# Kernel tuning notes

Measured on AMD Instinct MI355X. Metric: run time of the kernel, lower is better.

Reference implementation:

```python
import jax, jax.numpy as jnp
import numpy as np

N, F, H = 512, 256, 512

def _w(k, i, o):
    return jax.random.normal(k, (i, o), jnp.float32) * (1.0 / np.sqrt(i))

def setup_inputs() -> dict:
    key = jax.random.key(0)
    ks = jax.random.split(key, 12)
    z = lambda n: jnp.zeros((n,), jnp.float32)
    return {
        "node_features": jax.random.normal(ks[0], (N, F), jnp.float32),
        "adjacency": jax.random.uniform(ks[1], (N, N), jnp.float32),
        # GraphConv layers: neighbor linear (wl,bl) and self-loop (ws,bs)
        "gc1_wl": _w(ks[2], F, H), "gc1_bl": z(H), "gc1_ws": _w(ks[3], F, H), "gc1_bs": z(H),
        "gc2_wl": _w(ks[4], H, H), "gc2_bl": z(H), "gc2_ws": _w(ks[5], H, H), "gc2_bs": z(H),
        "gc3_wl": _w(ks[6], H, F), "gc3_bl": z(F), "gc3_ws": _w(ks[7], H, F), "gc3_bs": z(F),
        # edge MLP: Linear(2F,H) -> ReLU -> (dropout=identity, eval) -> Linear(H,H) -> ReLU -> Linear(H,1)
        "mlp_w1": _w(ks[8], 2 * F, H), "mlp_b1": z(H),
        "mlp_w2": _w(ks[9], H, H), "mlp_b2": z(H),
        "mlp_w3": _w(ks[10], H, 1), "mlp_b3": z(1),
    }

def _gconv(x, adj_norm, wl, bl, ws, bs):
    # adj_norm @ Linear(x) + SelfLoop(x)
    return adj_norm @ (x @ wl + bl) + (x @ ws + bs)

def reference(node_features, adjacency,
              gc1_wl, gc1_bl, gc1_ws, gc1_bs,
              gc2_wl, gc2_bl, gc2_ws, gc2_bs,
              gc3_wl, gc3_bl, gc3_ws, gc3_bs,
              mlp_w1, mlp_b1, mlp_w2, mlp_b2, mlp_w3, mlp_b3):
    # row-normalized adjacency (shared across all three layers)
    adj_norm = adjacency / (adjacency.sum(axis=1, keepdims=True) + 1e-8)
    x = jax.nn.relu(_gconv(node_features, adj_norm, gc1_wl, gc1_bl, gc1_ws, gc1_bs))
    x = jax.nn.relu(_gconv(x, adj_norm, gc2_wl, gc2_bl, gc2_ws, gc2_bs))
    emb = _gconv(x, adj_norm, gc3_wl, gc3_bl, gc3_ws, gc3_bs)  # [N, F]
    # vectorized all-pairs (i<j) edge scoring, symmetric scatter
    iu, ju = np.triu_indices(N, k=1)  # static index lists, P = N(N-1)/2
    ef = jnp.concatenate([emb[iu], emb[ju]], axis=-1)  # [P, 2F]
    h = jax.nn.relu(ef @ mlp_w1 + mlp_b1)
    h = jax.nn.relu(h @ mlp_w2 + mlp_b2)
    s = jax.nn.sigmoid((h @ mlp_w3 + mlp_b3)[:, 0])  # [P]
    edge_scores = jnp.zeros((N, N), emb.dtype).at[iu, ju].set(s).at[ju, iu].set(s)
    return emb, edge_scores
```

## Files before the change

### kernel.cpp

```cpp
#include <hip/hip_runtime.h>
#include <hip/hip_bf16.h>


#define NN 512
#define FF 256
#define HH 512

typedef __attribute__((ext_vector_type(8))) short s8v;
typedef __attribute__((ext_vector_type(4))) float f4v;

__device__ __forceinline__ ushort f2bf(float f) {
  unsigned u = __float_as_uint(f);
  unsigned r = (u + 0x7fffu + ((u >> 16) & 1u)) >> 16;
  return (ushort)r;
}

__global__ __launch_bounds__(256)
void rownorm_kernel(const float* __restrict__ adj, float* __restrict__ adjn) {
  int row = blockIdx.x;
  int tid = threadIdx.x;
  const float* r = adj + row * NN;
  float a0 = r[tid], a1 = r[tid + 256];
  float s = a0 + a1;
#pragma unroll
  for (int m = 1; m < 64; m <<= 1) s += __shfl_xor(s, m);
  __shared__ float wsum[4];
  if ((tid & 63) == 0) wsum[tid >> 6] = s;
  __syncthreads();
  float inv = 1.f / (wsum[0] + wsum[1] + wsum[2] + wsum[3] + 1e-8f);
  float* o = adjn + row * NN;
  o[tid] = a0 * inv;
  o[tid + 256] = a1 * inv;
}

template <bool RELU>
__global__ __launch_bounds__(256)
void gemm_ts(int M, int N, int K,
             const float* __restrict__ A, int lda,
             const float* __restrict__ B0, const float* __restrict__ B1, int ldb,
             const float* __restrict__ bias0, const float* __restrict__ bias1,
             const float* __restrict__ add0, const float* __restrict__ add1, int ldadd,
             float* __restrict__ C0, float* __restrict__ C1, int ldc)
{
  const float* B = blockIdx.z ? B1 : B0;
  const float* bias = blockIdx.z ? bias1 : bias0;
  const float* add = blockIdx.z ? add1 : add0;
  float* C = blockIdx.z ? C1 : C0;
  const int n0 = blockIdx.x * 64;
  const int m0 = blockIdx.y * 16;
  const int tid = threadIdx.x;
  const int ty = tid >> 4, tx = tid & 15;

  __shared__ float As[32][18];
  __shared__ float Bs[32][68];
  float4 acc = {0.f, 0.f, 0.f, 0.f};

  const int am = tid >> 4;
  const int ak = tid & 15;
  const int bk = tid >> 4;
  const int bn = tid & 15;

  float2 pa = *(const float2*)&A[(m0 + am) * lda + ak * 2];
  float4 pb0 = *(const float4*)&B[bk * ldb + n0 + bn * 4];
  float4 pb1 = *(const float4*)&B[(bk + 16) * ldb + n0 + bn * 4];

  for (int k0 = 0; k0 < K; k0 += 32) {
    As[ak * 2][am] = pa.x;
    As[ak * 2 + 1][am] = pa.y;
    *(float4*)&Bs[bk][bn * 4] = pb0;
    *(float4*)&Bs[bk + 16][bn * 4] = pb1;
    __syncthreads();
    if (k0 + 32 < K) {
      pa = *(const float2*)&A[(m0 + am) * lda + k0 + 32 + ak * 2];
      pb0 = *(const float4*)&B[(k0 + 32 + bk) * ldb + n0 + bn * 4];
      pb1 = *(const float4*)&B[(k0 + 48 + bk) * ldb + n0 + bn * 4];
    }
#pragma unroll
    for (int k = 0; k < 32; ++k) {
      float a = As[k][ty];
      float4 b = *(const float4*)&Bs[k][tx * 4];
      acc.x += a * b.x; acc.y += a * b.y; acc.z += a * b.z; acc.w += a * b.w;
    }
    __syncthreads();
  }

  int m = m0 + ty;
  float4 v = acc;
  if (bias) {
    float4 bv = *(const float4*)&bias[n0 + tx * 4];
    v.x += bv.x; v.y += bv.y; v.z += bv.z; v.w += bv.w;
  }
  if (add) {
    float4 d = *(const float4*)&add[m * ldadd + n0 + tx * 4];
    v.x += d.x; v.y += d.y; v.z += d.z; v.w += d.w;
  }
  if (RELU) {
    v.x = fmaxf(v.x, 0.f); v.y = fmaxf(v.y, 0.f);
    v.z = fmaxf(v.z, 0.f); v.w = fmaxf(v.w, 0.f);
  }
  *(float4*)&C[m * ldc + n0 + tx * 4] = v;
}

__global__ __launch_bounds__(256)
void w2_pack(const float* __restrict__ w2, ushort* __restrict__ w2t2) {
  int slab = blockIdx.y;
  int col = blockIdx.x * 64 + (threadIdx.x >> 2);
  int kq = threadIdx.x & 3;
  int k0 = slab * 32 + kq * 8;
  ushort tmp[8];
#pragma unroll
  for (int e = 0; e < 8; ++e) tmp[e] = f2bf(w2[(k0 + e) * HH + col]);
  ushort* dst = w2t2 + slab * 16384 + col * 32 + kq * 8;
  *(ushort4*)dst = *(ushort4*)tmp;
  *(ushort4*)(dst + 4) = *(ushort4*)&tmp[4];
}

__global__ __launch_bounds__(512)
__attribute__((amdgpu_waves_per_eu(2, 2)))
void edge_mlp(const float* __restrict__ Amat, const float* __restrict__ Bmat,
              const ushort* __restrict__ w2t2,
              const float* __restrict__ b2, const float* __restrict__ w3,
              const float* __restrict__ b3,
              float* __restrict__ edges)
{
  __shared__ ushort h1s[2][128 * 128];
  __shared__ float part[8][640];

  const int tb = (int)blockIdx.x;
  int bj = (int)((sqrtf(4.f * tb + 1.f) - 1.f) * 0.5f);
  while (bj * bj + bj > tb) --bj;
  while ((bj + 1) * (bj + 2) <= tb) ++bj;
  const int bi = tb - bj * bj - bj;

  const int tid = threadIdx.x;
  const int wid = tid >> 6;
  const int lane = tid & 63;
  const int l15 = lane & 15;
  const int lg = lane >> 4;

  const f4v zero = {0.f, 0.f, 0.f, 0.f};
  f4v acc[8][4];
#pragma unroll
  for (int mf = 0; mf < 8; ++mf)
#pragma unroll
    for (int nf = 0; nf < 4; ++nf) acc[mf][nf] = zero;

  auto stage = [&](int ch, int buf) {
#pragma unroll 2
    for (int q = 0; q < 8; ++q) {
      int fidx = q * 512 + tid;
      int p = fidx >> 5;
      int k4 = fidx & 31;
      int i = bi * 8 + (p >> 4);
      int j = bj * 16 + (p & 15);
      float4 av = *(const float4*)(Amat + i * HH + ch * 128 + k4 * 4);
      float4 bv = *(const float4*)(Bmat + j * HH + ch * 128 + k4 * 4);
      ushort4 pk;
      pk.x = f2bf(fmaxf(av.x + bv.x, 0.f));
      pk.y = f2bf(fmaxf(av.y + bv.y, 0.f));
      pk.z = f2bf(fmaxf(av.z + bv.z, 0.f));
      pk.w = f2bf(fmaxf(av.w + bv.w, 0.f));
      int off = (p * 256 + k4 * 8) ^ ((p & 7) << 4);
      *(ushort4*)((char*)h1s[buf] + off) = pk;
    }
  };

  stage(0, 0);
  __syncthreads();

  const ushort* wbase = w2t2 + wid * 2048 + l15 * 32 + lg * 8;

  for (int ch = 0; ch < 4; ++ch) {
    int cur = ch & 1;
    if (ch < 3) stage(ch + 1, cur ^ 1);
    s8v nb0, nb1, nb2, nb3;
    {
      const ushort* wb = wbase + (ch * 4) * 16384;
      nb0 = *(const s8v*)wb;
      nb1 = *(const s8v*)(wb + 512);
      nb2 = *(const s8v*)(wb + 1024);
      nb3 = *(const s8v*)(wb + 1536);
    }
#pragma unroll
    for (int ks = 0; ks < 4; ++ks) {
      s8v cb0 = nb0, cb1 = nb1, cb2 = nb2, cb3 = nb3;
      if (ks < 3) {
        const ushort* wb = wbase + (ch * 4 + ks + 1) * 16384;
        nb0 = *(const s8v*)wb;
        nb1 = *(const s8v*)(wb + 512);
        nb2 = *(const s8v*)(wb + 1024);
        nb3 = *(const s8v*)(wb + 1536);
      }
#pragma unroll
      for (int mf = 0; mf < 8; ++mf) {
        int p = mf * 16 + l15;
        int off = (p * 256 + ks * 64 + lg * 16) ^ ((p & 7) << 4);
        s8v a = *(const s8v*)((const char*)h1s[cur] + off);
        acc[mf][0] = __builtin_amdgcn_mfma_f32_16x16x32_bf16(a, cb0, acc[mf][0], 0, 0, 0);
        acc[mf][1] = __builtin_amdgcn_mfma_f32_16x16x32_bf16(a, cb1, acc[mf][1], 0, 0, 0);
        acc[mf][2] = __builtin_amdgcn_mfma_f32_16x16x32_bf16(a, cb2, acc[mf][2], 0, 0, 0);
        acc[mf][3] = __builtin_amdgcn_mfma_f32_16x16x32_bf16(a, cb3, acc[mf][3], 0, 0, 0);
      }
    }
    __syncthreads();
  }

  float bb[4], ww[4];
#pragma unroll
  for (int nf = 0; nf < 4; ++nf) {
    int col = wid * 64 + nf * 16 + l15;
    bb[nf] = b2[col];
    ww[nf] = w3[col];
  }
#pragma unroll
  for (int mf = 0; mf < 8; ++mf) {
    float ps[4];
#pragma unroll
    for (int e = 0; e < 4; ++e) {
      ps[e] = fmaxf(acc[mf][0][e] + bb[0], 0.f) * ww[0] +
              fmaxf(acc[mf][1][e] + bb[1], 0.f) * ww[1] +
              fmaxf(acc[mf][2][e] + bb[2], 0.f) * ww[2] +
              fmaxf(acc[mf][3][e] + bb[3], 0.f) * ww[3];
    }
#pragma unroll
    for (int m = 1; m < 16; m <<= 1) {
#pragma unroll
      for (int e = 0; e < 4; ++e) ps[e] += __shfl_xor(ps[e], m);
    }
    if (l15 == 0) {
#pragma unroll
      for (int e = 0; e < 4; ++e)
        part[wid][mf * 16 + lg * 4 + e] = ps[e];
    }
  }
  __syncthreads();
  if (tid < 128) {
    float tot = b3[0];
#pragma unroll
    for (int w = 0; w < 8; ++w) tot += part[w][tid];
    float sg = 1.f / (1.f + expf(-tot));
    int i = bi * 8 + (tid >> 4);
    int j = bj * 16 + (tid & 15);
    if (i < j) {
      edges[i * NN + j] = sg;
      edges[j * NN + i] = sg;
    } else if (i == j) {
      edges[i * NN + i] = 0.f;
    }
  }
}

extern "C" void kernel_launch(void* const* d_in, const int* in_sizes, int n_in,
                              void* d_out, int out_size, void* d_ws, size_t ws_size,
                              hipStream_t stream) {
  const float* node = (const float*)d_in[0];
  const float* adj  = (const float*)d_in[1];
  const float* g1wl = (const float*)d_in[2];
  const float* g1bl = (const float*)d_in[3];
  const float* g1ws = (const float*)d_in[4];
  const float* g1bs = (const float*)d_in[5];
  const float* g2wl = (const float*)d_in[6];
  const float* g2bl = (const float*)d_in[7];
  const float* g2ws = (const float*)d_in[8];
  const float* g2bs = (const float*)d_in[9];
  const float* g3wl = (const float*)d_in[10];
  const float* g3bl = (const float*)d_in[11];
  const float* g3ws = (const float*)d_in[12];
  const float* g3bs = (const float*)d_in[13];
  const float* w1 = (const float*)d_in[14];
  const float* b1 = (const float*)d_in[15];
  const float* w2 = (const float*)d_in[16];
  const float* b2 = (const float*)d_in[17];
  const float* w3 = (const float*)d_in[18];
  const float* b3 = (const float*)d_in[19];

  float* out = (float*)d_out;
  float* emb = out;
  float* edges = out + NN * FF;

  char* wsb = (char*)d_ws;
  float* adjn = (float*)wsb;
  float* Tb   = (float*)(wsb + (1u << 20));
  float* Sb   = (float*)(wsb + (2u << 20));
  float* xa   = (float*)(wsb + (3u << 20));
  float* xb   = (float*)(wsb + (4u << 20));
  ushort* w2t2 = (ushort*)(wsb + (5u << 20));
  float* Amat = Tb;
  float* Bmat = Sb;

  rownorm_kernel<<<NN, 256, 0, stream>>>(adj, adjn);
  w2_pack<<<dim3(8, 16), 256, 0, stream>>>(w2, w2t2);

  gemm_ts<false><<<dim3(8, 32, 2), 256, 0, stream>>>(
      NN, HH, FF, node, FF, g1wl, g1ws, HH, g1bl, g1bs,
      nullptr, nullptr, 0, Tb, Sb, HH);
  gemm_ts<true><<<dim3(8, 32, 1), 256, 0, stream>>>(
      NN, HH, NN, adjn, NN, Tb, Tb, HH, nullptr, nullptr,
      Sb, Sb, HH, xa, xa, HH);
  gemm_ts<false><<<dim3(8, 32, 2), 256, 0, stream>>>(
      NN, HH, HH, xa, HH, g2wl, g2ws, HH, g2bl, g2bs,
      nullptr, nullptr, 0, Tb, Sb, HH);
  gemm_ts<true><<<dim3(8, 32, 1), 256, 0, stream>>>(
      NN, HH, NN, adjn, NN, Tb, Tb, HH, nullptr, nullptr,
      Sb, Sb, HH, xb, xb, HH);
  gemm_ts<false><<<dim3(4, 32, 2), 256, 0, stream>>>(
      NN, FF, HH, xb, HH, g3wl, g3ws, FF, g3bl, g3bs,
      nullptr, nullptr, 0, Tb, Sb, FF);
  gemm_ts<false><<<dim3(4, 32, 1), 256, 0, stream>>>(
      NN, FF, NN, adjn, NN, Tb, Tb, FF, nullptr, nullptr,
      Sb, Sb, FF, emb, emb, FF);

  gemm_ts<false><<<dim3(8, 32, 2), 256, 0, stream>>>(
      NN, HH, FF, emb, FF, w1, w1 + FF * HH, HH, b1, nullptr,
      nullptr, nullptr, 0, Amat, Bmat, HH);

  edge_mlp<<<1056, 512, 0, stream>>>(Amat, Bmat, w2t2, b2, w3, b3, edges);
}
```

Before: 208.0 us.

## Split staging of next chunk into halves interleaved with MFMA slabs

The staging of the next h1 chunk (global loads of A/B rows, add+ReLU, bf16 pack, LDS store) is split into two halves. Each half's global loads are issued before two MFMA slab steps and written to LDS afterward, so load latency is hidden behind matrix math. The W2 prefetch now runs as a single chain across all 16 slabs instead of restarting per chunk. The extra float4 staging registers raise register pressure and may lower occupancy.

```diff
diff --git a/kernel.cpp b/kernel.cpp
--- a/kernel.cpp
+++ b/kernel.cpp
@@ -145,63 +145,81 @@
 #pragma unroll
     for (int nf = 0; nf < 4; ++nf) acc[mf][nf] = zero;
 
-  auto stage = [&](int ch, int buf) {
-#pragma unroll 2
-    for (int q = 0; q < 8; ++q) {
-      int fidx = q * 512 + tid;
+  float4 sa[4], sb[4];
+  auto issue_half = [&](int ch, int h) {
+#pragma unroll
+    for (int q = 0; q < 4; ++q) {
+      int fidx = (h * 4 + q) * 512 + tid;
       int p = fidx >> 5;
       int k4 = fidx & 31;
       int i = bi * 8 + (p >> 4);
       int j = bj * 16 + (p & 15);
-      float4 av = *(const float4*)(Amat + i * HH + ch * 128 + k4 * 4);
-      float4 bv = *(const float4*)(Bmat + j * HH + ch * 128 + k4 * 4);
+      sa[q] = *(const float4*)(Amat + i * HH + ch * 128 + k4 * 4);
+      sb[q] = *(const float4*)(Bmat + j * HH + ch * 128 + k4 * 4);
+    }
+  };
+  auto write_half = [&](int buf, int h) {
+#pragma unroll
+    for (int q = 0; q < 4; ++q) {
+      int fidx = (h * 4 + q) * 512 + tid;
+      int p = fidx >> 5;
+      int k4 = fidx & 31;
       ushort4 pk;
-      pk.x = f2bf(fmaxf(av.x + bv.x, 0.f));
-      pk.y = f2bf(fmaxf(av.y + bv.y, 0.f));
-      pk.z = f2bf(fmaxf(av.z + bv.z, 0.f));
-      pk.w = f2bf(fmaxf(av.w + bv.w, 0.f));
+      pk.x = f2bf(fmaxf(sa[q].x + sb[q].x, 0.f));
+      pk.y = f2bf(fmaxf(sa[q].y + sb[q].y, 0.f));
+      pk.z = f2bf(fmaxf(sa[q].z + sb[q].z, 0.f));
+      pk.w = f2bf(fmaxf(sa[q].w + sb[q].w, 0.f));
       int off = (p * 256 + k4 * 8) ^ ((p & 7) << 4);
       *(ushort4*)((char*)h1s[buf] + off) = pk;
     }
   };
 
-  stage(0, 0);
+  issue_half(0, 0); write_half(0, 0);
+  issue_half(0, 1); write_half(0, 1);
   __syncthreads();
 
   const ushort* wbase = w2t2 + wid * 2048 + l15 * 32 + lg * 8;
 
-  for (int ch = 0; ch < 4; ++ch) {
-    int cur = ch & 1;
-    if (ch < 3) stage(ch + 1, cur ^ 1);
-    s8v nb0, nb1, nb2, nb3;
-    {
-      const ushort* wb = wbase + (ch * 4) * 16384;
+  s8v nb0, nb1, nb2, nb3;
+  nb0 = *(const s8v*)wbase;
+  nb1 = *(const s8v*)(wbase + 512);
+  nb2 = *(const s8v*)(wbase + 1024);
+  nb3 = *(const s8v*)(wbase + 1536);
+
+  auto slab_step = [&](int cur, int slab) {
+    s8v cb0 = nb0, cb1 = nb1, cb2 = nb2, cb3 = nb3;
+    if (slab < 15) {
+      const ushort* wb = wbase + (slab + 1) * 16384;
       nb0 = *(const s8v*)wb;
       nb1 = *(const s8v*)(wb + 512);
       nb2 = *(const s8v*)(wb + 1024);
       nb3 = *(const s8v*)(wb + 1536);
     }
-#pragma unroll
-    for (int ks = 0; ks < 4; ++ks) {
-      s8v cb0 = nb0, cb1 = nb1, cb2 = nb2, cb3 = nb3;
-      if (ks < 3) {
-        const ushort* wb = wbase + (ch * 4 + ks + 1) * 16384;
-        nb0 = *(const s8v*)wb;
-        nb1 = *(const s8v*)(wb + 512);
-        nb2 = *(const s8v*)(wb + 1024);
-        nb3 = *(const s8v*)(wb + 1536);
-      }
-#pragma unroll
-      for (int mf = 0; mf < 8; ++mf) {
-        int p = mf * 16 + l15;
-        int off = (p * 256 + ks * 64 + lg * 16) ^ ((p & 7) << 4);
-        s8v a = *(const s8v*)((const char*)h1s[cur] + off);
-        acc[mf][0] = __builtin_amdgcn_mfma_f32_16x16x32_bf16(a, cb0, acc[mf][0], 0, 0, 0);
-        acc[mf][1] = __builtin_amdgcn_mfma_f32_16x16x32_bf16(a, cb1, acc[mf][1], 0, 0, 0);
-        acc[mf][2] = __builtin_amdgcn_mfma_f32_16x16x32_bf16(a, cb2, acc[mf][2], 0, 0, 0);
-        acc[mf][3] = __builtin_amdgcn_mfma_f32_16x16x32_bf16(a, cb3, acc[mf][3], 0, 0, 0);
-      }
-    }
+    int ks = slab & 3;
+#pragma unroll
+    for (int mf = 0; mf < 8; ++mf) {
+      int p = mf * 16 + l15;
+      int off = (p * 256 + ks * 64 + lg * 16) ^ ((p & 7) << 4);
+      s8v a = *(const s8v*)((const char*)h1s[cur] + off);
+      acc[mf][0] = __builtin_amdgcn_mfma_f32_16x16x32_bf16(a, cb0, acc[mf][0], 0, 0, 0);
+      acc[mf][1] = __builtin_amdgcn_mfma_f32_16x16x32_bf16(a, cb1, acc[mf][1], 0, 0, 0);
+      acc[mf][2] = __builtin_amdgcn_mfma_f32_16x16x32_bf16(a, cb2, acc[mf][2], 0, 0, 0);
+      acc[mf][3] = __builtin_amdgcn_mfma_f32_16x16x32_bf16(a, cb3, acc[mf][3], 0, 0, 0);
+    }
+  };
+
+  for (int ch = 0; ch < 4; ++ch) {
+    int cur = ch & 1;
+    if (ch < 3) issue_half(ch + 1, 0);
+    slab_step(cur, ch * 4 + 0);
+    slab_step(cur, ch * 4 + 1);
+    if (ch < 3) {
+      write_half(cur ^ 1, 0);
+      issue_half(ch + 1, 1);
+    }
+    slab_step(cur, ch * 4 + 2);
+    slab_step(cur, ch * 4 + 3);
+    if (ch < 3) write_half(cur ^ 1, 1);
     __syncthreads();
   }
 
```

Result: faster. 194.3 us (-6.6%).
